# Kernel optimization log

Measured on AMD Instinct MI355X. Metric: run time of the kernel, lower is better.

The kernel has to match this reference:

```python
import jax, jax.numpy as jnp
import numpy as np

KERNEL = 25
TOP_K = 8

def _decomp(x, kernel=KERNEL):
    # x: (B,T,D); replicate-pad along time, moving-average via cumsum
    pad = (kernel - 1) // 2
    xp = jnp.pad(x, ((0, 0), (pad, pad), (0, 0)), mode='edge')
    cs = jnp.cumsum(xp, axis=1)
    cs = jnp.concatenate([jnp.zeros_like(cs[:, :1]), cs], axis=1)
    trend = (cs[:, kernel:] - cs[:, :-kernel]) / kernel  # (B,T,D)
    return x - trend, trend

def _autocorrelation(x, Wq, bq, Wk, bk, Wv, bv, top_k=TOP_K):
    B, T, D = x.shape
    q = x @ Wq + bq
    k = x @ Wk + bk
    v = x @ Wv + bv
    nfft = 1 << int(2 * T - 1).bit_length()
    fq = jnp.fft.rfft(q, n=nfft, axis=1)
    fk = jnp.fft.rfft(k, n=nfft, axis=1)
    corr = jnp.fft.irfft(fq * jnp.conj(fk), n=nfft, axis=1)[:, :T]  # (B,T,D)
    score = corr.mean(axis=-1)  # (B,T)
    score = score.at[:, 0].set(-1e9)
    K = min(top_k, T - 1)
    _, lags = jax.lax.top_k(score, K)  # (B,K) int32
    t = jnp.arange(T)

    def shift_add(acc, lag):  # lag: (B,)
        idx = (t[None, :] - lag[:, None]) % T          # (B,T)
        shifted = jax.vmap(lambda vb, ib: vb[ib])(v, idx)  # (B,T,D)
        return acc + shifted, None

    out, _ = jax.lax.scan(shift_add, jnp.zeros_like(v), lags.T)
    return out / K

def setup_inputs() -> dict:
    key = jax.random.key(0)
    ks = jax.random.split(key, 8)
    B, T, D, F = 16, 2048, 512, 2048
    s = 0.02
    return {
        'x':  jax.random.normal(ks[0], (B, T, D), jnp.float32),
        'Wq': jax.random.normal(ks[1], (D, D), jnp.float32) * s,
        'bq': jnp.zeros((D,), jnp.float32),
        'Wk': jax.random.normal(ks[2], (D, D), jnp.float32) * s,
        'bk': jnp.zeros((D,), jnp.float32),
        'Wv': jax.random.normal(ks[3], (D, D), jnp.float32) * s,
        'bv': jnp.zeros((D,), jnp.float32),
        'W1': jax.random.normal(ks[4], (D, F), jnp.float32) * s,
        'b1': jnp.zeros((F,), jnp.float32),
        'W2': jax.random.normal(ks[5], (F, D), jnp.float32) * s,
        'b2': jnp.zeros((D,), jnp.float32),
    }

def reference(x, Wq, bq, Wk, bk, Wv, bv, W1, b1, W2, b2):
    seasonal, trend1 = _decomp(x)
    seasonal = seasonal + _autocorrelation(seasonal, Wq, bq, Wk, bk, Wv, bv)
    seasonal, trend2 = _decomp(seasonal)
    h = jax.nn.gelu(seasonal @ W1 + b1, approximate=False)  # torch GELU is exact erf
    seasonal = seasonal + (h @ W2 + b2)
    trend = trend1 + trend2
    return seasonal, trend
```

## Files before the change

### kernel.cpp

```cpp
#include <hip/hip_runtime.h>
#include <hip/hip_fp8.h>
#include <cstdint>
#include <cstddef>

#define NB 16
#define T_ 2048
#define D_ 512
#define F_ 2048

using f16 = _Float16;
typedef __attribute__((ext_vector_type(8))) f16 f16x8;
typedef __attribute__((ext_vector_type(4))) f16 f16x4;
typedef __attribute__((ext_vector_type(4))) float f32x4;
typedef __attribute__((ext_vector_type(2))) long longx2;

__device__ __forceinline__ void g2l16(const void* g, void* l) {
  __builtin_amdgcn_global_load_lds((const __attribute__((address_space(1))) void*)g,
                                   (__attribute__((address_space(3))) void*)l,
                                   16, 0, 0);
}

__device__ __forceinline__ unsigned char to_fp8(float v) {
  __hip_fp8_e4m3 q(v);
  return (unsigned char)q.__x;
}

__device__ __forceinline__ float gelu_fast(float x) {
  float z = fabsf(x) * 0.70710678118654752f;
  float t = 1.f / (1.f + 0.3275911f * z);
  float poly = t*(0.254829592f + t*(-0.284496736f + t*(1.421413741f +
               t*(-1.453152027f + t*1.061405429f))));
  float e = __expf(-z*z);
  float er = 1.f - poly*e;
  er = copysignf(er, x);
  return 0.5f * x * (1.f + er);
}

template<int EPI>
__global__ __launch_bounds__(512, 4) void gemm_kernel(
    const f16* __restrict__ A, int lda,
    const f16* __restrict__ Bt, int ldb,
    void* __restrict__ Cv, int ldc,
    const float* __restrict__ bias, int K, int nN)
{
  __shared__ __align__(16) char smem[73728];

  const int nwg = gridDim.x, wg = blockIdx.x;
  const int cpx = nwg >> 3;
  const int swz = (wg & 7)*cpx + (wg >> 3);
  const int n0 = (swz % nN) * 256;
  const int m0 = (swz / nN) * 128;

  const int tid = threadIdx.x;
  const int w = tid >> 6, lane = tid & 63;

  const int oA = tid*16;
  const int rowAs = oA >> 6;
  const size_t gAo = (size_t)rowAs*lda + ((((oA>>4)&3) ^ ((rowAs>>1)&3))*8);
  int oB[2]; size_t gBo[2];
  #pragma unroll
  for (int i = 0; i < 2; ++i) {
    int o = i*8192 + tid*16;
    int row = o >> 6;
    int ss = ((o >> 4) & 3) ^ ((row >> 1) & 3);
    oB[i] = o;
    gBo[i] = (size_t)row*ldb + ss*8;
  }
  const f16* Ab = A  + (size_t)m0*lda;
  const f16* Bb = Bt + (size_t)n0*ldb;

  auto stage = [&](int t) {
    const f16* As = Ab + t*32;
    const f16* Bs = Bb + t*32;
    char* dst = smem + (t % 3)*24576;
    g2l16(As + gAo, dst + oA);
    #pragma unroll
    for (int i = 0; i < 2; ++i)
      g2l16(Bs + gBo[i], dst + 8192 + oB[i]);
  };

  const int wm = w >> 2, wn = w & 3;
  const int lr = lane & 15, ks = lane >> 4;
  int offA[4], offB[4];
  #pragma unroll
  for (int i = 0; i < 4; ++i) {
    int rowA = wm*64 + i*16 + lr;
    int rowB = wn*64 + i*16 + lr;
    offA[i] = rowA*64 + ((ks ^ ((rowA >> 1) & 3)) << 4);
    offB[i] = rowB*64 + ((ks ^ ((rowB >> 1) & 3)) << 4);
  }

  f32x4 acc[4][4];
  #pragma unroll
  for (int i = 0; i < 4; ++i)
    #pragma unroll
    for (int j = 0; j < 4; ++j) acc[i][j] = f32x4{0.f, 0.f, 0.f, 0.f};

  const int nk = K >> 5;
  stage(0); stage(1);

  for (int t = 0; t < nk; ++t) {
    if (t + 1 < nk) { asm volatile("s_waitcnt vmcnt(3)" ::: "memory"); }
    else            { asm volatile("s_waitcnt vmcnt(0)" ::: "memory"); }
    __builtin_amdgcn_s_barrier();
    const char* pA = (const char*)smem + (t % 3)*24576;
    const char* pB = pA + 8192;
    f16x8 af[4], bf[4];
    #pragma unroll
    for (int i = 0; i < 4; ++i) {
      af[i] = *(const f16x8*)(pA + offA[i]);
      bf[i] = *(const f16x8*)(pB + offB[i]);
    }
    if (t + 2 < nk) stage(t + 2);
    #pragma unroll
    for (int mi = 0; mi < 4; ++mi)
      #pragma unroll
      for (int ni = 0; ni < 4; ++ni)
        acc[mi][ni] = __builtin_amdgcn_mfma_f32_16x16x32_f16(af[mi], bf[ni], acc[mi][ni], 0, 0, 0);
    __builtin_amdgcn_s_barrier();
  }

  const int lq = lane >> 4;
  #pragma unroll
  for (int mi = 0; mi < 4; ++mi) {
    #pragma unroll
    for (int ni = 0; ni < 4; ++ni) {
      int col = wn*64 + ni*16 + lr;
      float bv = bias[n0 + col];
      int slot = col >> 3, cb = (col & 7) << 1;
      #pragma unroll
      for (int r = 0; r < 4; ++r) {
        float val = acc[mi][ni][r] + bv;
        int row = wm*64 + mi*16 + lq*4 + r;
        *(f16*)(smem + row*512 + ((slot ^ (row & 31)) << 4) + cb) = (f16)val;
      }
    }
  }
  __syncthreads();
  f16* Ch = (f16*)Cv;
  #pragma unroll
  for (int it2 = 0; it2 < 8; ++it2) {
    int row = (tid >> 5) + it2*16;
    int s = tid & 31;
    f16x8 vv = *(const f16x8*)(smem + row*512 + ((s ^ (row & 31)) << 4));
    *(f16x8*)&Ch[(size_t)(m0 + row)*ldc + n0 + s*8] = vv;
  }
}

template<int EPI>
__global__ __launch_bounds__(512, 4) void gemm8_kernel(
    const unsigned char* __restrict__ A, int lda,
    const unsigned char* __restrict__ Bt, int ldb,
    void* __restrict__ Cv, int ldc,
    const float* __restrict__ bias, int K, int nN,
    float sIn, float sOut, const f16* __restrict__ S2)
{
  __shared__ __align__(16) char smem[73728];

  const int nwg = gridDim.x, wg = blockIdx.x;
  const int cpx = nwg >> 3;
  const int swz = (wg & 7)*cpx + (wg >> 3);
  const int n0 = (swz % nN) * 256;
  const int m0 = (swz / nN) * 128;

  const int tid = threadIdx.x;
  const int w = tid >> 6, lane = tid & 63;

  const int oA = tid*16;
  const int rowAs = oA >> 6;
  const size_t gAo = (size_t)rowAs*lda + ((((oA>>4)&3) ^ ((rowAs>>1)&3)) << 4);
  int oB[2]; size_t gBo[2];
  #pragma unroll
  for (int i = 0; i < 2; ++i) {
    int o = i*8192 + tid*16;
    int row = o >> 6;
    int ss = ((o >> 4) & 3) ^ ((row >> 1) & 3);
    oB[i] = o;
    gBo[i] = (size_t)row*ldb + (ss << 4);
  }
  const unsigned char* Ab = A  + (size_t)m0*lda;
  const unsigned char* Bb = Bt + (size_t)n0*ldb;

  auto stage = [&](int t) {
    const unsigned char* As = Ab + t*64;
    const unsigned char* Bs = Bb + t*64;
    char* dst = smem + (t % 3)*24576;
    g2l16(As + gAo, dst + oA);
    #pragma unroll
    for (int i = 0; i < 2; ++i)
      g2l16(Bs + gBo[i], dst + 8192 + oB[i]);
  };

  const int wm = w >> 2, wn = w & 3;
  const int lr = lane & 15, ks = lane >> 4;
  int offA8[4], offB8[4];
  #pragma unroll
  for (int i = 0; i < 4; ++i) {
    int rowA = wm*64 + i*16 + lr;
    int rowB = wn*64 + i*16 + lr;
    offA8[i] = rowA*64 + ((ks ^ ((rowA >> 1) & 3)) << 4);
    offB8[i] = rowB*64 + ((ks ^ ((rowB >> 1) & 3)) << 4);
  }

  f32x4 acc[4][4];
  #pragma unroll
  for (int i = 0; i < 4; ++i)
    #pragma unroll
    for (int j = 0; j < 4; ++j) acc[i][j] = f32x4{0.f, 0.f, 0.f, 0.f};

  const int nk = K >> 6;
  stage(0); stage(1);

  for (int t = 0; t < nk; ++t) {
    if (t + 1 < nk) { asm volatile("s_waitcnt vmcnt(3)" ::: "memory"); }
    else            { asm volatile("s_waitcnt vmcnt(0)" ::: "memory"); }
    __builtin_amdgcn_s_barrier();
    const char* pA = (const char*)smem + (t % 3)*24576;
    const char* pB = pA + 8192;
    longx2 av[4], bv[4];
    #pragma unroll
    for (int i = 0; i < 4; ++i) {
      av[i] = *(const longx2*)(pA + offA8[i]);
      bv[i] = *(const longx2*)(pB + offB8[i]);
    }
    if (t + 2 < nk) stage(t + 2);
    #pragma unroll
    for (int mi = 0; mi < 4; ++mi)
      #pragma unroll
      for (int ni = 0; ni < 4; ++ni)
        acc[mi][ni] = __builtin_amdgcn_mfma_f32_16x16x32_fp8_fp8(av[mi][0], bv[ni][0], acc[mi][ni], 0, 0, 0);
    #pragma unroll
    for (int mi = 0; mi < 4; ++mi)
      #pragma unroll
      for (int ni = 0; ni < 4; ++ni)
        acc[mi][ni] = __builtin_amdgcn_mfma_f32_16x16x32_fp8_fp8(av[mi][1], bv[ni][1], acc[mi][ni], 0, 0, 0);
    __builtin_amdgcn_s_barrier();
  }

  const int lq = lane >> 4;
  if (EPI == 1) {
    #pragma unroll
    for (int mi = 0; mi < 4; ++mi) {
      #pragma unroll
      for (int ni = 0; ni < 4; ++ni) {
        int col = wn*64 + ni*16 + lr;
        float bv = bias[n0 + col];
        int slot = col >> 3, cb = (col & 7) << 1;
        #pragma unroll
        for (int r = 0; r < 4; ++r) {
          float val = sOut * gelu_fast(acc[mi][ni][r]*sIn + bv);
          int row = wm*64 + mi*16 + lq*4 + r;
          *(f16*)(smem + row*512 + ((slot ^ (row & 31)) << 4) + cb) = (f16)val;
        }
      }
    }
    __syncthreads();
    unsigned char* Ch = (unsigned char*)Cv;
    #pragma unroll
    for (int it2 = 0; it2 < 8; ++it2) {
      int row = (tid >> 5) + it2*16;
      int s = tid & 31;
      f16x8 vv = *(const f16x8*)(smem + row*512 + ((s ^ (row & 31)) << 4));
      int lo = 0, hi = 0;
      lo = __builtin_amdgcn_cvt_pk_fp8_f32((float)vv[0], (float)vv[1], lo, false);
      lo = __builtin_amdgcn_cvt_pk_fp8_f32((float)vv[2], (float)vv[3], lo, true);
      hi = __builtin_amdgcn_cvt_pk_fp8_f32((float)vv[4], (float)vv[5], hi, false);
      hi = __builtin_amdgcn_cvt_pk_fp8_f32((float)vv[6], (float)vv[7], hi, true);
      unsigned long long pk = ((unsigned long long)(unsigned int)hi << 32)
                            | (unsigned int)lo;
      int dcol = (s >> 3)*64 + 16*(s & 3) + 8*((s >> 2) & 1);
      *(unsigned long long*)&Ch[(size_t)(m0 + row)*ldc + n0 + dcol] = pk;
    }
  } else {
    float* Cf = (float*)Cv;
    #pragma unroll
    for (int p = 0; p < 2; ++p) {
      __syncthreads();
      if (wm == p) {
        #pragma unroll
        for (int mi = 0; mi < 4; ++mi) {
          #pragma unroll
          for (int ni = 0; ni < 4; ++ni) {
            int col = wn*64 + ni*16 + lr;
            float bv = bias[n0 + col];
            int slot = col >> 2, cb = (col & 3) << 2;
            #pragma unroll
            for (int r = 0; r < 4; ++r) {
              float val = acc[mi][ni][r]*sIn + bv;
              int row = mi*16 + lq*4 + r;
              *(float*)(smem + row*1024 + ((slot ^ (row & 63)) << 4) + cb) = val;
            }
          }
        }
      }
      __syncthreads();
      #pragma unroll
      for (int it2 = 0; it2 < 8; ++it2) {
        int row = (tid >> 6) + it2*8;
        int s = tid & 63;
        f32x4 vv = *(const f32x4*)(smem + row*1024 + ((s ^ (row & 63)) << 4));
        size_t o = (size_t)(m0 + p*64 + row)*ldc + n0 + s*4;
        f16x4 s2 = *(const f16x4*)&S2[o];
        f32x4 outv;
        #pragma unroll
        for (int j = 0; j < 4; ++j) outv[j] = vv[j] + (float)s2[j];
        *(f32x4*)&Cf[o] = outv;
      }
    }
  }
}

__device__ __forceinline__ void diag_epilogue2(float* ctile, f32x4 (&acc)[4][4],
                                               int dg, int b, float* __restrict__ score)
{
  const int tid = threadIdx.x;
  const int w = tid >> 6, lane = tid & 63;
  const int wm = w >> 1, wn = w & 1, lr = lane & 15, lq = lane >> 4;
  float total = 0.f;
  #pragma unroll
  for (int pass = 0; pass < 2; ++pass) {
    __builtin_amdgcn_s_barrier();
    if (wn == pass) {
      #pragma unroll
      for (int mi = 0; mi < 4; ++mi) {
        #pragma unroll
        for (int ni = 0; ni < 4; ++ni) {
          int colL = ni*16 + lr;
          int row0 = wm*64 + mi*16 + lq*4;
          *(f32x4*)(&ctile[colL*128 + row0]) = acc[mi][ni];
        }
      }
    }
    asm volatile("s_waitcnt lgkmcnt(0)" ::: "memory");
    __builtin_amdgcn_s_barrier();
    if (tid < 255) {
      int delta = tid - 127;
      #pragma unroll 8
      for (int cc = 0; cc < 64; ++cc) {
        int r = pass*64 + cc + delta;
        if ((unsigned)r < 128u) total += ctile[cc*128 + r];
      }
    }
    asm volatile("s_waitcnt lgkmcnt(0)" ::: "memory");
  }
  __builtin_amdgcn_s_barrier();
  if (tid < 255) {
    int tau = dg*128 + (tid - 127);
    if (tau >= 1 && tau < T_) atomicAdd(&score[(size_t)b*T_ + tau], total);
  }
}

__global__ __launch_bounds__(256, 2) void score2_kernel(
    const f16* __restrict__ xact, const f16* __restrict__ z,
    float* __restrict__ score)
{
  __shared__ __align__(16) f16 stage[3*8192];
  __shared__ float ctile[64*128];

  const int b = blockIdx.x, h = blockIdx.y, g = blockIdx.z;
  const int tid = threadIdx.x;
  const int w = tid >> 6, lane = tid & 63;

  const int o0 = (w*2+0)*1024 + lane*16;
  const int o1 = (w*2+1)*1024 + lane*16;
  const int r0 = o0 >> 6, r1 = o1 >> 6;
  const int s0 = ((o0>>4)&3) ^ ((r0>>1)&3);
  const int s1 = ((o1>>4)&3) ^ ((r1>>1)&3);
  const size_t gq0 = (size_t)r0*512  + s0*8,  gq1 = (size_t)r1*512  + s1*8;
  const size_t gk0 = (size_t)r0*1024 + s0*8,  gk1 = (size_t)r1*1024 + s1*8;
  const int l0 = (w*2+0)*512, l1 = (w*2+1)*512;

  const int nA = 16 - g;
  const int nsteps = 17*4;
  const int groupA_end = nA*4;

  const int wm = w >> 1, wn = w & 1;
  const int lr = lane & 15, ks = lane >> 4;
  int offQ[4], offK[4];
  #pragma unroll
  for (int i = 0; i < 4; ++i) {
    int row = wm*64 + i*16 + lr;
    offQ[i] = row*64 + ((ks ^ ((row>>1)&3)) << 4);
    int col = wn*64 + i*16 + lr;
    offK[i] = col*64 + ((ks ^ ((col>>1)&3)) << 4);
  }

  auto issue = [&](int sp) {
    int p = sp >> 2, kt = sp & 3;
    int ti, tj;
    if (p < nA) { tj = p; ti = p + g; }
    else        { tj = p - nA; ti = tj + 15 - g; }
    size_t qb = ((size_t)(b*T_ + ti*128))*512  + h*128 + kt*32;
    size_t kb = ((size_t)(b*T_ + tj*128))*1024 + h*128 + kt*32;
    f16* dst = stage + (sp % 3)*8192;
    g2l16(xact + qb + gq0, dst + l0);
    g2l16(xact + qb + gq1, dst + l1);
    g2l16(z + kb + gk0, dst + 4096 + l0);
    g2l16(z + kb + gk1, dst + 4096 + l1);
  };

  f32x4 acc[4][4];
  #pragma unroll
  for (int i = 0; i < 4; ++i)
    #pragma unroll
    for (int j = 0; j < 4; ++j) acc[i][j] = f32x4{0.f, 0.f, 0.f, 0.f};

  issue(0);
  issue(1);

  for (int sp = 0; sp < nsteps; ++sp) {
    if (sp + 1 < nsteps) { asm volatile("s_waitcnt vmcnt(4)" ::: "memory"); }
    else                 { asm volatile("s_waitcnt vmcnt(0)" ::: "memory"); }
    __builtin_amdgcn_s_barrier();
    const char* base = (const char*)stage + (sp % 3)*16384;
    f16x8 af[4], bf[4];
    #pragma unroll
    for (int i = 0; i < 4; ++i) {
      af[i] = *(const f16x8*)(base + offQ[i]);
      bf[i] = *(const f16x8*)(base + 8192 + offK[i]);
    }
    if (sp + 2 < nsteps) issue(sp + 2);
    #pragma unroll
    for (int mi = 0; mi < 4; ++mi)
      #pragma unroll
      for (int ni = 0; ni < 4; ++ni)
        acc[mi][ni] = __builtin_amdgcn_mfma_f32_16x16x32_f16(af[mi], bf[ni], acc[mi][ni], 0, 0, 0);
    __builtin_amdgcn_s_barrier();
    if (sp == groupA_end - 1) {
      diag_epilogue2(ctile, acc, g, b, score);
      #pragma unroll
      for (int i = 0; i < 4; ++i)
        #pragma unroll
        for (int j = 0; j < 4; ++j) acc[i][j] = f32x4{0.f, 0.f, 0.f, 0.f};
    }
  }
  diag_epilogue2(ctile, acc, 15 - g, b, score);
}

__global__ void topk_kernel(const float* __restrict__ score, int* __restrict__ lags)
{
  const int b = blockIdx.x, tid = threadIdx.x;
  __shared__ float vals[T_];
  __shared__ float rmax[256];
  __shared__ int   rarg[256];
  __shared__ int   outk[8];
  for (int t = tid; t < T_; t += 256) vals[t] = (t == 0) ? -1e30f : score[(size_t)b*T_ + t];
  __syncthreads();
  for (int k = 0; k < 8; ++k) {
    float m = -1e30f; int mi = 0x7fffffff;
    for (int t = tid; t < T_; t += 256) {
      float v = vals[t];
      if (v > m || (v == m && t < mi)) { m = v; mi = t; }
    }
    rmax[tid] = m; rarg[tid] = mi;
    __syncthreads();
    for (int s = 128; s > 0; s >>= 1) {
      if (tid < s) {
        float v2 = rmax[tid+s]; int i2 = rarg[tid+s];
        if (v2 > rmax[tid] || (v2 == rmax[tid] && i2 < rarg[tid])) { rmax[tid] = v2; rarg[tid] = i2; }
      }
      __syncthreads();
    }
    if (tid == 0) { outk[k] = rarg[0]; vals[rarg[0]] = -1e30f; }
    __syncthreads();
  }
  if (tid < 8) lags[b*8 + tid] = outk[tid];
}

__global__ void decomp1_kernel(const float* __restrict__ x,
                               f16* __restrict__ t1_16, f16* __restrict__ s16)
{
  int idx = blockIdx.x*256 + threadIdx.x;
  int d4 = idx & 127, t = (idx >> 7) & (T_-1), b = idx >> 18;
  const float* xb = x + ((size_t)b*T_)*D_ + d4*4;
  f32x4 sum = {0.f,0.f,0.f,0.f};
  f32x4 center = {0.f,0.f,0.f,0.f};
  #pragma unroll
  for (int j = -12; j <= 12; ++j) {
    int tt = t + j; tt = tt < 0 ? 0 : (tt > T_-1 ? T_-1 : tt);
    f32x4 v = *(const f32x4*)(xb + (size_t)tt*D_);
    sum += v;
    if (j == 0) center = v;
  }
  f32x4 tr = sum * (1.f/25.f);
  size_t o = ((size_t)(b*T_ + t))*D_ + d4*4;
  f16x4 tv;
  #pragma unroll
  for (int i = 0; i < 4; ++i) tv[i] = (f16)tr[i];
  *(f16x4*)(t1_16 + o) = tv;
  f32x4 s = center - tr;
  f16x4 hv;
  #pragma unroll
  for (int i = 0; i < 4; ++i) hv[i] = (f16)s[i];
  *(f16x4*)(s16 + o) = hv;
}

__global__ void decomp2_kernel(const f16* __restrict__ sac,
                               const f16* __restrict__ t1_16,
                               float* __restrict__ trend_out,
                               unsigned char* __restrict__ s2_8,
                               f16* __restrict__ s2_16)
{
  int idx = blockIdx.x*256 + threadIdx.x;
  int d4 = idx & 127, t = (idx >> 7) & (T_-1), b = idx >> 18;
  const f16* sb = sac + ((size_t)b*T_)*D_ + d4*4;
  f32x4 sum = {0.f,0.f,0.f,0.f};
  f32x4 center = {0.f,0.f,0.f,0.f};
  #pragma unroll
  for (int j = -12; j <= 12; ++j) {
    int tt = t + j; tt = tt < 0 ? 0 : (tt > T_-1 ? T_-1 : tt);
    f16x4 v = *(const f16x4*)(sb + (size_t)tt*D_);
    f32x4 vf = { (float)v[0], (float)v[1], (float)v[2], (float)v[3] };
    sum += vf;
    if (j == 0) center = vf;
  }
  f32x4 tr = sum * (1.f/25.f);
  size_t o = ((size_t)(b*T_ + t))*D_ + d4*4;
  f32x4 s = center - tr;
  f16x4 hv;
  #pragma unroll
  for (int i = 0; i < 4; ++i) hv[i] = (f16)s[i];
  *(f16x4*)(s2_16 + o) = hv;
  int c0 = d4*4;
  int q = (c0 & 63) >> 3;
  int dcol = (c0 >> 6)*64 + 16*(q & 3) + 8*(q >> 2) + (c0 & 7);
  int pk = 0;
  pk = __builtin_amdgcn_cvt_pk_fp8_f32(s[0], s[1], pk, false);
  pk = __builtin_amdgcn_cvt_pk_fp8_f32(s[2], s[3], pk, true);
  *(unsigned int*)(s2_8 + ((size_t)(b*T_ + t))*D_ + dcol) = pk;
  f16x4 t1 = *(const f16x4*)(t1_16 + o);
  f32x4 tot;
  #pragma unroll
  for (int i = 0; i < 4; ++i) tot[i] = (float)t1[i] + tr[i];
  *(f32x4*)(trend_out + o) = tot;
}

__global__ void gather_kernel(const f16* __restrict__ zv, f16* __restrict__ act,
                              const int* __restrict__ lags)
{
  int idx = blockIdx.x*256 + threadIdx.x;
  int d8 = idx & 63, t = (idx >> 6) & (T_-1), b = idx >> 17;
  const f16* vb = zv + (size_t)b*T_*1024 + 512 + d8*8;
  f16* ap = act + ((size_t)(b*T_ + t))*D_ + d8*8;
  f16x8 s = *(const f16x8*)ap;
  float a[8];
  #pragma unroll
  for (int j = 0; j < 8; ++j) a[j] = (float)s[j];
  #pragma unroll
  for (int k = 0; k < 8; ++k) {
    int lag = lags[b*8 + k];
    int tt = (t - lag + T_) & (T_-1);
    f16x8 v = *(const f16x8*)(vb + (size_t)tt*1024);
    #pragma unroll
    for (int j = 0; j < 8; ++j) a[j] += 0.125f * (float)v[j];
  }
  f16x8 o;
  #pragma unroll
  for (int j = 0; j < 8; ++j) o[j] = (f16)a[j];
  *(f16x8*)ap = o;
}

__global__ void prepack_kernel(const float* __restrict__ Wq, const float* __restrict__ Wk,
                               const float* __restrict__ Wv, const float* __restrict__ bv,
                               const float* __restrict__ W1, const float* __restrict__ W2,
                               f16* __restrict__ wq16, f16* __restrict__ wk16,
                               f16* __restrict__ zvw, unsigned char* __restrict__ w1p,
                               unsigned char* __restrict__ w2p, float* __restrict__ bcat)
{
  int i = blockIdx.x*256 + threadIdx.x;
  if (i < 262144) {
    wq16[i] = (f16)Wq[i];
  } else if (i < 524288) {
    int j = i - 262144;
    wk16[j] = (f16)Wk[j];
  } else if (i < 786432) {
    int j = i - 524288;
    int n = j >> 9, k = j & 511;
    zvw[262144 + j] = (f16)Wv[k*512 + n];
  } else if (i < 1835008) {
    int j = i - 786432;
    int n = j >> 9, jk = j & 511;
    int k = (jk & ~63) + (jk & 7) + 8*((jk >> 4) & 3) + 32*((jk >> 3) & 1);
    w1p[j] = to_fp8(16.f * W1[k*2048 + n]);
  } else if (i < 2883584) {
    int j = i - 1835008;
    int n = j >> 11, jk = j & 2047;
    int k = (jk & ~63) + (jk & 7) + 8*((jk >> 4) & 3) + 32*((jk >> 3) & 1);
    w2p[j] = to_fp8(16.f * W2[k*512 + n]);
  } else if (i < 2884608) {
    int j = i - 2883584;
    bcat[j] = j < 512 ? 0.f : bv[j - 512];
  }
}

extern "C" void kernel_launch(void* const* d_in, const int* in_sizes, int n_in,
                              void* d_out, int out_size, void* d_ws, size_t ws_size,
                              hipStream_t stream)
{
  const float* x  = (const float*)d_in[0];
  const float* Wq = (const float*)d_in[1];
  const float* Wk = (const float*)d_in[3];
  const float* Wv = (const float*)d_in[5];
  const float* bv = (const float*)d_in[6];
  const float* W1 = (const float*)d_in[7];
  const float* b1 = (const float*)d_in[8];
  const float* W2 = (const float*)d_in[9];
  const float* b2 = (const float*)d_in[10];

  float* out_seas  = (float*)d_out;
  float* out_trend = out_seas + (size_t)NB*T_*D_;

  char* ws = (char*)d_ws;
  f16*   act0  = (f16*)(ws);
  f16*   zv    = (f16*)(ws + 33554432ull);
  unsigned char* s2_8 = (unsigned char*)(ws + 33554432ull);
  f16*   s2_16 = (f16*)(ws + 50331648ull);
  unsigned char* h8   = (unsigned char*)(ws + 100663296ull);
  f16*   t1_16 = (f16*)(ws + 167772160ull);
  f16*   wq16  = (f16*)(ws + 201326592ull);
  f16*   wk16  = (f16*)(ws + 201851904ull);
  f16*   zvw   = (f16*)(ws + 202377216ull);
  unsigned char* w1p = (unsigned char*)(ws + 203425792ull);
  unsigned char* w2p = (unsigned char*)(ws + 204474368ull);
  float* bcat  = (float*)(ws + 205522944ull);
  float* score = (float*)(ws + 205529088ull);
  int*   lags  = (int*)(ws + 205660160ull);

  (void)hipMemsetAsync(score, 0, (size_t)NB*T_*sizeof(float), stream);
  prepack_kernel<<<11268, 256, 0, stream>>>(Wq, Wk, Wv, bv, W1, W2,
                                            wq16, wk16, zvw, w1p, w2p, bcat);
  decomp1_kernel<<<NB*T_*(D_/4)/256, 256, 0, stream>>>(x, t1_16, act0);
  gemm_kernel<0><<<8, 512, 0, stream>>>(wq16, 512, wk16, 512, zvw, 512, bcat, 512, 2);
  gemm_kernel<0><<<1024, 512, 0, stream>>>(act0, 512, zvw, 512, zv, 1024, bcat, 512, 4);
  score2_kernel<<<dim3(16, 4, 8), 256, 0, stream>>>(act0, zv, score);
  topk_kernel<<<NB, 256, 0, stream>>>(score, lags);
  gather_kernel<<<NB*T_*(D_/8)/256, 256, 0, stream>>>(zv, act0, lags);
  decomp2_kernel<<<NB*T_*(D_/4)/256, 256, 0, stream>>>(act0, t1_16, out_trend, s2_8, s2_16);
  gemm8_kernel<1><<<2048, 512, 0, stream>>>(s2_8, 512, w1p, 512, h8, 2048, b1,
                                            512, 8, 1.f/16.f, 8.f, nullptr);
  gemm8_kernel<2><<<512, 512, 0, stream>>>(h8, 2048, w2p, 2048, out_seas, 512, b2,
                                           2048, 2, 1.f/128.f, 1.f, s2_16);
}
```

Before: 486.5 us.

## Use sliding-window running sums in decomposition kernels and cheaper erf approximation

Both decomposition kernels now give each thread a chunk of 128 consecutive time steps and keep a running window sum, instead of each thread re-summing 25 rows. Each output row then costs two loads and an add rather than 25 loads. This cuts the launch to 128 blocks of 256 threads, so parallelism drops sharply and each thread does a long serial loop. The GELU erf approximation is also swapped for a lower-order 3-term polynomial, which is cheaper but less accurate.

```diff
diff --git a/kernel.cpp b/kernel.cpp
--- a/kernel.cpp
+++ b/kernel.cpp
@@ -27,11 +27,9 @@
 
 __device__ __forceinline__ float gelu_fast(float x) {
   float z = fabsf(x) * 0.70710678118654752f;
-  float t = 1.f / (1.f + 0.3275911f * z);
-  float poly = t*(0.254829592f + t*(-0.284496736f + t*(1.421413741f +
-               t*(-1.453152027f + t*1.061405429f))));
-  float e = __expf(-z*z);
-  float er = 1.f - poly*e;
+  float t = 1.f / (1.f + 0.47047f * z);
+  float poly = t*(0.3480242f + t*(-0.0958798f + t*0.7478556f));
+  float er = 1.f - poly * __expf(-z*z);
   er = copysignf(er, x);
   return 0.5f * x * (1.f + er);
 }
@@ -470,29 +468,29 @@
 __global__ void decomp1_kernel(const float* __restrict__ x,
                                f16* __restrict__ t1_16, f16* __restrict__ s16)
 {
-  int idx = blockIdx.x*256 + threadIdx.x;
-  int d4 = idx & 127, t = (idx >> 7) & (T_-1), b = idx >> 18;
+  int id = blockIdx.x*256 + threadIdx.x;
+  int d4 = id & 127, chunk = (id >> 7) & 15, b = id >> 11;
   const float* xb = x + ((size_t)b*T_)*D_ + d4*4;
-  f32x4 sum = {0.f,0.f,0.f,0.f};
-  f32x4 center = {0.f,0.f,0.f,0.f};
-  #pragma unroll
-  for (int j = -12; j <= 12; ++j) {
-    int tt = t + j; tt = tt < 0 ? 0 : (tt > T_-1 ? T_-1 : tt);
-    f32x4 v = *(const f32x4*)(xb + (size_t)tt*D_);
-    sum += v;
-    if (j == 0) center = v;
-  }
-  f32x4 tr = sum * (1.f/25.f);
-  size_t o = ((size_t)(b*T_ + t))*D_ + d4*4;
-  f16x4 tv;
-  #pragma unroll
-  for (int i = 0; i < 4; ++i) tv[i] = (f16)tr[i];
-  *(f16x4*)(t1_16 + o) = tv;
-  f32x4 s = center - tr;
-  f16x4 hv;
-  #pragma unroll
-  for (int i = 0; i < 4; ++i) hv[i] = (f16)s[i];
-  *(f16x4*)(s16 + o) = hv;
+  auto ld = [&](int t) -> f32x4 {
+    t = t < 0 ? 0 : (t > T_-1 ? T_-1 : t);
+    return *(const f32x4*)(xb + (size_t)t*D_);
+  };
+  const int t0 = chunk*128;
+  f32x4 W = {0.f,0.f,0.f,0.f};
+  #pragma unroll
+  for (int j = -12; j <= 12; ++j) W += ld(t0 + j);
+  for (int t = t0; t < t0 + 128; ++t) {
+    f32x4 c = ld(t);
+    f32x4 tr = W * (1.f/25.f);
+    f32x4 s = c - tr;
+    size_t o = ((size_t)(b*T_ + t))*D_ + d4*4;
+    f16x4 tv, hv;
+    #pragma unroll
+    for (int i = 0; i < 4; ++i) { tv[i] = (f16)tr[i]; hv[i] = (f16)s[i]; }
+    *(f16x4*)(t1_16 + o) = tv;
+    *(f16x4*)(s16 + o) = hv;
+    W += ld(t + 13) - ld(t - 12);
+  }
 }
 
 __global__ void decomp2_kernel(const f16* __restrict__ sac,
@@ -501,38 +499,41 @@
                                unsigned char* __restrict__ s2_8,
                                f16* __restrict__ s2_16)
 {
-  int idx = blockIdx.x*256 + threadIdx.x;
-  int d4 = idx & 127, t = (idx >> 7) & (T_-1), b = idx >> 18;
+  int id = blockIdx.x*256 + threadIdx.x;
+  int d4 = id & 127, chunk = (id >> 7) & 15, b = id >> 11;
   const f16* sb = sac + ((size_t)b*T_)*D_ + d4*4;
-  f32x4 sum = {0.f,0.f,0.f,0.f};
-  f32x4 center = {0.f,0.f,0.f,0.f};
-  #pragma unroll
-  for (int j = -12; j <= 12; ++j) {
-    int tt = t + j; tt = tt < 0 ? 0 : (tt > T_-1 ? T_-1 : tt);
-    f16x4 v = *(const f16x4*)(sb + (size_t)tt*D_);
-    f32x4 vf = { (float)v[0], (float)v[1], (float)v[2], (float)v[3] };
-    sum += vf;
-    if (j == 0) center = vf;
-  }
-  f32x4 tr = sum * (1.f/25.f);
-  size_t o = ((size_t)(b*T_ + t))*D_ + d4*4;
-  f32x4 s = center - tr;
-  f16x4 hv;
-  #pragma unroll
-  for (int i = 0; i < 4; ++i) hv[i] = (f16)s[i];
-  *(f16x4*)(s2_16 + o) = hv;
-  int c0 = d4*4;
-  int q = (c0 & 63) >> 3;
-  int dcol = (c0 >> 6)*64 + 16*(q & 3) + 8*(q >> 2) + (c0 & 7);
-  int pk = 0;
-  pk = __builtin_amdgcn_cvt_pk_fp8_f32(s[0], s[1], pk, false);
-  pk = __builtin_amdgcn_cvt_pk_fp8_f32(s[2], s[3], pk, true);
-  *(unsigned int*)(s2_8 + ((size_t)(b*T_ + t))*D_ + dcol) = pk;
-  f16x4 t1 = *(const f16x4*)(t1_16 + o);
-  f32x4 tot;
-  #pragma unroll
-  for (int i = 0; i < 4; ++i) tot[i] = (float)t1[i] + tr[i];
-  *(f32x4*)(trend_out + o) = tot;
+  auto ld = [&](int t) -> f32x4 {
+    t = t < 0 ? 0 : (t > T_-1 ? T_-1 : t);
+    f16x4 v = *(const f16x4*)(sb + (size_t)t*D_);
+    return f32x4{(float)v[0], (float)v[1], (float)v[2], (float)v[3]};
+  };
+  const int c0 = d4*4;
+  const int q = (c0 & 63) >> 3;
+  const int dcol = (c0 >> 6)*64 + 16*(q & 3) + 8*(q >> 2) + (c0 & 7);
+  const int t0 = chunk*128;
+  f32x4 W = {0.f,0.f,0.f,0.f};
+  #pragma unroll
+  for (int j = -12; j <= 12; ++j) W += ld(t0 + j);
+  for (int t = t0; t < t0 + 128; ++t) {
+    f32x4 c = ld(t);
+    f32x4 tr = W * (1.f/25.f);
+    f32x4 s = c - tr;
+    size_t o = ((size_t)(b*T_ + t))*D_ + d4*4;
+    f16x4 hv;
+    #pragma unroll
+    for (int i = 0; i < 4; ++i) hv[i] = (f16)s[i];
+    *(f16x4*)(s2_16 + o) = hv;
+    int pk = 0;
+    pk = __builtin_amdgcn_cvt_pk_fp8_f32(s[0], s[1], pk, false);
+    pk = __builtin_amdgcn_cvt_pk_fp8_f32(s[2], s[3], pk, true);
+    *(unsigned int*)(s2_8 + ((size_t)(b*T_ + t))*D_ + dcol) = pk;
+    f16x4 t1 = *(const f16x4*)(t1_16 + o);
+    f32x4 tot;
+    #pragma unroll
+    for (int i = 0; i < 4; ++i) tot[i] = (float)t1[i] + tr[i];
+    *(f32x4*)(trend_out + o) = tot;
+    W += ld(t + 13) - ld(t - 12);
+  }
 }
 
 __global__ void gather_kernel(const f16* __restrict__ zv, f16* __restrict__ act,
@@ -629,13 +630,13 @@
   (void)hipMemsetAsync(score, 0, (size_t)NB*T_*sizeof(float), stream);
   prepack_kernel<<<11268, 256, 0, stream>>>(Wq, Wk, Wv, bv, W1, W2,
                                             wq16, wk16, zvw, w1p, w2p, bcat);
-  decomp1_kernel<<<NB*T_*(D_/4)/256, 256, 0, stream>>>(x, t1_16, act0);
+  decomp1_kernel<<<128, 256, 0, stream>>>(x, t1_16, act0);
   gemm_kernel<0><<<8, 512, 0, stream>>>(wq16, 512, wk16, 512, zvw, 512, bcat, 512, 2);
   gemm_kernel<0><<<1024, 512, 0, stream>>>(act0, 512, zvw, 512, zv, 1024, bcat, 512, 4);
   score2_kernel<<<dim3(16, 4, 8), 256, 0, stream>>>(act0, zv, score);
   topk_kernel<<<NB, 256, 0, stream>>>(score, lags);
   gather_kernel<<<NB*T_*(D_/8)/256, 256, 0, stream>>>(zv, act0, lags);
-  decomp2_kernel<<<NB*T_*(D_/4)/256, 256, 0, stream>>>(act0, t1_16, out_trend, s2_8, s2_16);
+  decomp2_kernel<<<128, 256, 0, stream>>>(act0, t1_16, out_trend, s2_8, s2_16);
   gemm8_kernel<1><<<2048, 512, 0, stream>>>(s2_8, 512, w1p, 512, h8, 2048, b1,
                                             512, 8, 1.f/16.f, 8.f, nullptr);
   gemm8_kernel<2><<<512, 512, 0, stream>>>(h8, 2048, w2p, 2048, out_seas, 512, b2,
```

Result: faster. 450.6 us, median of 2 (-7.4%).
